# Kernel tuning notes

Measured on AMD Instinct MI355X. Metric: run time of the kernel, lower is better.

The kernel has to match this reference:

```python
import jax, jax.numpy as jnp
import numpy as np

S, B_BOX, C = 7, 2, 20
LAMBDA_COORD = 5.0
LAMBDA_NOOBJ = 0.5


def _iou(b1, b2):
    # b1, b2: [..., 4] in (cx, cy, w, h) format
    area1 = b1[..., 2] * b1[..., 3]
    area2 = b2[..., 2] * b2[..., 3]
    max_left = jnp.maximum(b1[..., 0] - b1[..., 2] / 2, b2[..., 0] - b2[..., 2] / 2)
    min_right = jnp.minimum(b1[..., 0] + b1[..., 2] / 2, b2[..., 0] + b2[..., 2] / 2)
    max_top = jnp.maximum(b1[..., 1] - b1[..., 3] / 2, b2[..., 1] - b2[..., 3] / 2)
    min_bottom = jnp.minimum(b1[..., 1] + b1[..., 3] / 2, b2[..., 1] + b2[..., 3] / 2)
    iw = jnp.maximum(min_right - max_left, 0.0)
    ih = jnp.maximum(min_bottom - max_top, 0.0)
    inter = iw * ih
    union = area1 + area2 - inter
    return jnp.where(inter > 0.0, inter / union, 0.0)


def setup_inputs() -> dict:
    key = jax.random.key(0)
    k1, k2, k3 = jax.random.split(key, 3)
    batch = 16384
    shape = (batch, S, S, C + 5 * B_BOX)  # [..., 30]
    pred = jax.random.uniform(k1, shape, dtype=jnp.float32)
    target = jax.random.uniform(k2, shape, dtype=jnp.float32)
    # objectness flag must be exactly 1.0 to trigger the obj branch
    obj_flag = jax.random.bernoulli(k3, 0.3, shape[:-1]).astype(jnp.float32)
    target = target.at[..., 0].set(obj_flag)
    return {"pred": pred, "target": target}


def reference(pred, target):
    batch = pred.shape[0]
    pred = pred.reshape(-1, S, S, C + 5 * B_BOX)
    target = target.reshape(-1, S, S, C + 5 * B_BOX)

    obj = (target[..., 0] == 1.0)          # [b,S,S] bool
    obj_f = obj.astype(pred.dtype)
    noobj_f = 1.0 - obj_f

    gt = target[..., 1:5]
    box1 = pred[..., 1:5]                   # predictor 1 box
    box2 = target[..., 6:10]                # NOTE: original code uses target's 2nd box
    iou1 = jax.lax.stop_gradient(_iou(box1, gt))
    iou2 = jax.lax.stop_gradient(_iou(box2, gt))
    resp1 = iou1 > iou2                     # predictor 1 responsible (strict >)
    r1 = resp1[..., None]

    # coord losses (responsible predictor)
    pxy = jnp.where(r1, pred[..., 1:3], pred[..., 6:8])
    txy = jnp.where(r1, target[..., 1:3], target[..., 6:8])
    pwh = jnp.where(r1, pred[..., 3:5], pred[..., 8:10])
    twh = jnp.where(r1, target[..., 3:5], target[..., 8:10])
    cell_xy = jnp.sum((pxy - txy) ** 2, axis=-1)
    cell_wh = jnp.sum((jnp.sqrt(pwh) - jnp.sqrt(twh)) ** 2, axis=-1)

    # obj confidence loss: responsible conf vs its iou
    conf_resp = jnp.where(resp1, pred[..., 0], pred[..., 5])
    iou_resp = jnp.where(resp1, iou1, iou2)
    cell_obj = (conf_resp - iou_resp) ** 2

    # noobj: non-responsible conf in obj cells; both confs in empty cells
    conf_other = jnp.where(resp1, pred[..., 5], pred[..., 0])
    cell_noobj_obj = conf_other ** 2
    cell_noobj_empty = pred[..., 0] ** 2 + pred[..., 5] ** 2

    cell_class = jnp.sum((pred[..., 10:] - target[..., 10:]) ** 2, axis=-1)

    loss_coord_xy = LAMBDA_COORD * jnp.sum(obj_f * cell_xy)
    loss_coord_wh = LAMBDA_COORD * jnp.sum(obj_f * cell_wh)
    loss_obj = jnp.sum(obj_f * cell_obj)
    loss_noobj = LAMBDA_NOOBJ * (jnp.sum(obj_f * cell_noobj_obj) + jnp.sum(noobj_f * cell_noobj_empty))
    loss_class = jnp.sum(obj_f * cell_class)
    loss = loss_coord_xy + loss_coord_wh + loss_obj + loss_noobj + loss_class

    bs = jnp.asarray(batch, pred.dtype)
    return ((loss_coord_xy + loss_coord_wh) / bs,
            loss_obj / bs,
            loss_noobj / bs,
            loss_class / bs,
            loss / bs)
```

## Files before the change

kernel.cpp:

```cpp
#include <hip/hip_runtime.h>

#define NCH 30
#define F2PC 15
#define TILE 64
#define TPB 64
#define MAXB 2560

typedef float fvec2 __attribute__((ext_vector_type(2)));
typedef float fvec4 __attribute__((ext_vector_type(4)));

__device__ __forceinline__ float iou_fn(float x1, float y1, float w1, float h1,
                                        float x2, float y2, float w2, float h2) {
    float a1 = w1 * h1, a2 = w2 * h2;
    float left  = fmaxf(x1 - w1 * 0.5f, x2 - w2 * 0.5f);
    float right = fminf(x1 + w1 * 0.5f, x2 + w2 * 0.5f);
    float top   = fmaxf(y1 - h1 * 0.5f, y2 - h2 * 0.5f);
    float bot   = fminf(y1 + h1 * 0.5f, y2 + h2 * 0.5f);
    float iw = fmaxf(right - left, 0.0f);
    float ih = fmaxf(bot - top, 0.0f);
    float inter = iw * ih;
    float uni = a1 + a2 - inter;
    return (inter > 0.0f) ? (inter / uni) : 0.0f;
}

__device__ __forceinline__ void cell_losses(const float* p, const float* t,
                                            float& coord, float& lobj,
                                            float& lnoobj, float& lclass) {
    float obj_f = (t[0] == 1.0f) ? 1.0f : 0.0f;

    float iou1 = iou_fn(p[1], p[2], p[3], p[4], t[1], t[2], t[3], t[4]);
    float iou2 = iou_fn(t[6], t[7], t[8], t[9], t[1], t[2], t[3], t[4]);
    bool r = iou1 > iou2;

    float px = r ? p[1] : p[6], py = r ? p[2] : p[7];
    float pw = r ? p[3] : p[8], ph = r ? p[4] : p[9];
    float tx = r ? t[1] : t[6], ty = r ? t[2] : t[7];
    float tw = r ? t[3] : t[8], th = r ? t[4] : t[9];

    float dx = px - tx, dy = py - ty;
    float cxy = dx * dx + dy * dy;
    float swv = sqrtf(pw) - sqrtf(tw), shv = sqrtf(ph) - sqrtf(th);
    float cwh = swv * swv + shv * shv;

    float conf_resp  = r ? p[0] : p[5];
    float iou_resp   = r ? iou1 : iou2;
    float conf_other = r ? p[5] : p[0];
    float dconf = conf_resp - iou_resp;

    coord  += obj_f * (cxy + cwh);
    lobj   += obj_f * dconf * dconf;
    lnoobj += obj_f * conf_other * conf_other
            + (1.0f - obj_f) * (p[0] * p[0] + p[5] * p[5]);

    float cls = 0.0f;
#pragma unroll
    for (int i = 10; i < NCH; i++) { float e = p[i] - t[i]; cls += e * e; }
    lclass += obj_f * cls;
}

#define LOADT(RP, RT, RP7, RT7, tile_) do {                                              \
    const long long b4_ = (long long)(tile_) * 480;                                      \
    _Pragma("unroll")                                                                    \
    for (int k_ = 0; k_ < 7; k_++) {                                                     \
        RP[k_] = __builtin_nontemporal_load(reinterpret_cast<const fvec4*>(pred) + b4_ + k_ * 64 + lane); \
        RT[k_] = __builtin_nontemporal_load(reinterpret_cast<const fvec4*>(targ) + b4_ + k_ * 64 + lane); \
    }                                                                                    \
    RP7 = __builtin_nontemporal_load(reinterpret_cast<const fvec2*>(pred) + 2 * b4_ + 896 + lane); \
    RT7 = __builtin_nontemporal_load(reinterpret_cast<const fvec2*>(targ) + 2 * b4_ + 896 + lane); \
} while (0)

#define STORE_LDS(RP, RT, RP7, RT7) do {                                                 \
    _Pragma("unroll")                                                                    \
    for (int k_ = 0; k_ < 7; k_++) {                                                     \
        sp4[k_ * 64 + lane] = RP[k_];                                                    \
        st4[k_ * 64 + lane] = RT[k_];                                                    \
    }                                                                                    \
    reinterpret_cast<fvec2*>(sp4)[896 + lane] = RP7;                                     \
    reinterpret_cast<fvec2*>(st4)[896 + lane] = RT7;                                     \
} while (0)

#define COMPUTE() do {                                                                   \
    float p_[NCH], t_[NCH];                                                              \
    const fvec2* pp_ = reinterpret_cast<const fvec2*>(sp4) + lane * F2PC;                \
    const fvec2* tp_ = reinterpret_cast<const fvec2*>(st4) + lane * F2PC;                \
    _Pragma("unroll")                                                                    \
    for (int k_ = 0; k_ < F2PC; k_++) { fvec2 v_ = pp_[k_]; p_[2 * k_] = v_.x; p_[2 * k_ + 1] = v_.y; } \
    _Pragma("unroll")                                                                    \
    for (int k_ = 0; k_ < F2PC; k_++) { fvec2 v_ = tp_[k_]; t_[2 * k_] = v_.x; t_[2 * k_ + 1] = v_.y; } \
    cell_losses(p_, t_, coord, lobj, lnoobj, lclass);                                    \
} while (0)

__global__ __launch_bounds__(TPB) void yolo_main(
        const float* __restrict__ pred, const float* __restrict__ targ,
        float4* __restrict__ partials, int n_full, int n_cells) {
    __shared__ fvec4 sp4[TILE * F2PC / 2];
    __shared__ fvec4 st4[TILE * F2PC / 2];

    const int lane = threadIdx.x;
    float coord = 0.f, lobj = 0.f, lnoobj = 0.f, lclass = 0.f;

    fvec4 rpA[7], rtA[7]; fvec2 rpA7, rtA7;
    fvec4 rpB[7], rtB[7]; fvec2 rpB7, rtB7;

    const int stride = gridDim.x;
    int tc = blockIdx.x;

    if (tc < n_full)              LOADT(rpA, rtA, rpA7, rtA7, tc);
    if (tc + stride < n_full)     LOADT(rpB, rtB, rpB7, rtB7, tc + stride);

    for (;;) {
        if (tc >= n_full) break;
        __syncthreads();
        STORE_LDS(rpA, rtA, rpA7, rtA7);
        if (tc + 2 * stride < n_full)
            LOADT(rpA, rtA, rpA7, rtA7, tc + 2 * stride);
        __syncthreads();
        COMPUTE();
        tc += stride;

        if (tc >= n_full) break;
        __syncthreads();
        STORE_LDS(rpB, rtB, rpB7, rtB7);
        if (tc + 2 * stride < n_full)
            LOADT(rpB, rtB, rpB7, rtB7, tc + 2 * stride);
        __syncthreads();
        COMPUTE();
        tc += stride;
    }

    if (blockIdx.x == 0) {
        int cell = n_full * TILE + lane;
        if (cell < n_cells) {
            float p[NCH], tt[NCH];
            const fvec2* pp = reinterpret_cast<const fvec2*>(pred) + (long long)cell * F2PC;
            const fvec2* tp = reinterpret_cast<const fvec2*>(targ) + (long long)cell * F2PC;
#pragma unroll
            for (int k = 0; k < F2PC; k++) { fvec2 v = pp[k]; p[2 * k] = v.x; p[2 * k + 1] = v.y; }
#pragma unroll
            for (int k = 0; k < F2PC; k++) { fvec2 v = tp[k]; tt[2 * k] = v.x; tt[2 * k + 1] = v.y; }
            cell_losses(p, tt, coord, lobj, lnoobj, lclass);
        }
    }

#pragma unroll
    for (int off = 32; off > 0; off >>= 1) {
        coord  += __shfl_down(coord, off);
        lobj   += __shfl_down(lobj, off);
        lnoobj += __shfl_down(lnoobj, off);
        lclass += __shfl_down(lclass, off);
    }
    if (lane == 0) partials[blockIdx.x] = make_float4(coord, lobj, lnoobj, lclass);
}

__global__ __launch_bounds__(256) void yolo_reduce(
        const float4* __restrict__ partials, int nparts,
        float* __restrict__ out, double inv_bs) {
    double s0 = 0.0, s1 = 0.0, s2 = 0.0, s3 = 0.0;
    for (int i = threadIdx.x; i < nparts; i += 256) {
        float4 v = partials[i];
        s0 += (double)v.x; s1 += (double)v.y;
        s2 += (double)v.z; s3 += (double)v.w;
    }
#pragma unroll
    for (int off = 32; off > 0; off >>= 1) {
        s0 += __shfl_down(s0, off);
        s1 += __shfl_down(s1, off);
        s2 += __shfl_down(s2, off);
        s3 += __shfl_down(s3, off);
    }
    __shared__ double red[4][4];
    int lane = threadIdx.x & 63;
    int wid  = threadIdx.x >> 6;
    if (lane == 0) {
        red[wid][0] = s0; red[wid][1] = s1;
        red[wid][2] = s2; red[wid][3] = s3;
    }
    __syncthreads();
    if (threadIdx.x == 0) {
        double a0 = 0, a1 = 0, a2 = 0, a3 = 0;
        for (int w = 0; w < 4; w++) {
            a0 += red[w][0]; a1 += red[w][1];
            a2 += red[w][2]; a3 += red[w][3];
        }
        double cd = a0 * 5.0 * inv_bs;
        double o  = a1 * inv_bs;
        double n  = a2 * 0.5 * inv_bs;
        double cl = a3 * inv_bs;
        out[0] = (float)cd;
        out[1] = (float)o;
        out[2] = (float)n;
        out[3] = (float)cl;
        out[4] = (float)(cd + o + n + cl);
    }
}

extern "C" void kernel_launch(void* const* d_in, const int* in_sizes, int n_in,
                              void* d_out, int out_size, void* d_ws, size_t ws_size,
                              hipStream_t stream) {
    const float* pred = (const float*)d_in[0];
    const float* targ = (const float*)d_in[1];
    float* out = (float*)d_out;
    float4* partials = (float4*)d_ws;

    int n_cells = in_sizes[0] / NCH;
    int batch   = n_cells / 49;
    int n_full  = n_cells / TILE;

    int grid = (n_full < 1) ? 1 : (n_full < MAXB ? n_full : MAXB);

    int max_parts = (int)(ws_size / sizeof(float4));
    if (max_parts >= 1 && grid > max_parts) grid = max_parts;

    yolo_main<<<grid, TPB, 0, stream>>>(pred, targ, partials, n_full, n_cells);
    yolo_reduce<<<1, 256, 0, stream>>>(partials, grid, out, 1.0 / (double)batch);
}
```

Measured before the change: 196.0 us.

## Load tiles directly into LDS with global_load_lds and drop block barriers

Result: faster. 191.8 us (-2.2%).

```diff
diff --git a/kernel.cpp b/kernel.cpp
--- a/kernel.cpp
+++ b/kernel.cpp
@@ -4,7 +4,7 @@
 #define F2PC 15
 #define TILE 64
 #define TPB 64
-#define MAXB 2560
+#define MAXB 1280
 
 typedef float fvec2 __attribute__((ext_vector_type(2)));
 typedef float fvec4 __attribute__((ext_vector_type(4)));
@@ -58,31 +58,37 @@
     lclass += obj_f * cls;
 }
 
-#define LOADT(RP, RT, RP7, RT7, tile_) do {                                              \
+#define GLDS16(gp, lp)                                                                   \
+    __builtin_amdgcn_global_load_lds(                                                    \
+        (const __attribute__((address_space(1))) void*)(gp),                             \
+        (__attribute__((address_space(3))) void*)(lp), 16, 0, 2)
+
+#define ISSUE_TILE(buf, tile_) do {                                                      \
     const long long b4_ = (long long)(tile_) * 480;                                      \
+    const fvec4* gp_ = reinterpret_cast<const fvec4*>(pred) + b4_;                       \
+    const fvec4* gt_ = reinterpret_cast<const fvec4*>(targ) + b4_;                       \
     _Pragma("unroll")                                                                    \
     for (int k_ = 0; k_ < 7; k_++) {                                                     \
-        RP[k_] = __builtin_nontemporal_load(reinterpret_cast<const fvec4*>(pred) + b4_ + k_ * 64 + lane); \
-        RT[k_] = __builtin_nontemporal_load(reinterpret_cast<const fvec4*>(targ) + b4_ + k_ * 64 + lane); \
+        GLDS16(gp_ + k_ * 64 + lane, &sbuf[buf][0][k_ * 64]);                            \
+        GLDS16(gt_ + k_ * 64 + lane, &sbuf[buf][1][k_ * 64]);                            \
     }                                                                                    \
-    RP7 = __builtin_nontemporal_load(reinterpret_cast<const fvec2*>(pred) + 2 * b4_ + 896 + lane); \
-    RT7 = __builtin_nontemporal_load(reinterpret_cast<const fvec2*>(targ) + 2 * b4_ + 896 + lane); \
+    if (lane < 32) {                                                                     \
+        GLDS16(gp_ + 448 + lane, &sbuf[buf][0][448]);                                    \
+        GLDS16(gt_ + 448 + lane, &sbuf[buf][1][448]);                                    \
+    }                                                                                    \
 } while (0)
 
-#define STORE_LDS(RP, RT, RP7, RT7) do {                                                 \
-    _Pragma("unroll")                                                                    \
-    for (int k_ = 0; k_ < 7; k_++) {                                                     \
-        sp4[k_ * 64 + lane] = RP[k_];                                                    \
-        st4[k_ * 64 + lane] = RT[k_];                                                    \
-    }                                                                                    \
-    reinterpret_cast<fvec2*>(sp4)[896 + lane] = RP7;                                     \
-    reinterpret_cast<fvec2*>(st4)[896 + lane] = RT7;                                     \
-} while (0)
-
-#define COMPUTE() do {                                                                   \
+#define WAITV16 do { asm volatile("s_waitcnt vmcnt(16)" ::: "memory"); \
+                     __builtin_amdgcn_sched_barrier(0); } while (0)
+#define WAITV0  do { asm volatile("s_waitcnt vmcnt(0)"  ::: "memory"); \
+                     __builtin_amdgcn_sched_barrier(0); } while (0)
+#define LDS_REUSE_GUARD do { asm volatile("s_waitcnt lgkmcnt(0)" ::: "memory"); \
+                             __builtin_amdgcn_sched_barrier(0); } while (0)
+
+#define COMPUTE(buf) do {                                                                \
     float p_[NCH], t_[NCH];                                                              \
-    const fvec2* pp_ = reinterpret_cast<const fvec2*>(sp4) + lane * F2PC;                \
-    const fvec2* tp_ = reinterpret_cast<const fvec2*>(st4) + lane * F2PC;                \
+    const fvec2* pp_ = reinterpret_cast<const fvec2*>(&sbuf[buf][0][0]) + lane * F2PC;   \
+    const fvec2* tp_ = reinterpret_cast<const fvec2*>(&sbuf[buf][1][0]) + lane * F2PC;   \
     _Pragma("unroll")                                                                    \
     for (int k_ = 0; k_ < F2PC; k_++) { fvec2 v_ = pp_[k_]; p_[2 * k_] = v_.x; p_[2 * k_ + 1] = v_.y; } \
     _Pragma("unroll")                                                                    \
@@ -93,38 +99,30 @@
 __global__ __launch_bounds__(TPB) void yolo_main(
         const float* __restrict__ pred, const float* __restrict__ targ,
         float4* __restrict__ partials, int n_full, int n_cells) {
-    __shared__ fvec4 sp4[TILE * F2PC / 2];
-    __shared__ fvec4 st4[TILE * F2PC / 2];
+    __shared__ fvec4 sbuf[2][2][480];
 
     const int lane = threadIdx.x;
     float coord = 0.f, lobj = 0.f, lnoobj = 0.f, lclass = 0.f;
 
-    fvec4 rpA[7], rtA[7]; fvec2 rpA7, rtA7;
-    fvec4 rpB[7], rtB[7]; fvec2 rpB7, rtB7;
-
     const int stride = gridDim.x;
     int tc = blockIdx.x;
 
-    if (tc < n_full)              LOADT(rpA, rtA, rpA7, rtA7, tc);
-    if (tc + stride < n_full)     LOADT(rpB, rtB, rpB7, rtB7, tc + stride);
+    if (tc < n_full)          ISSUE_TILE(0, tc);
+    if (tc + stride < n_full) ISSUE_TILE(1, tc + stride);
 
     for (;;) {
         if (tc >= n_full) break;
-        __syncthreads();
-        STORE_LDS(rpA, rtA, rpA7, rtA7);
-        if (tc + 2 * stride < n_full)
-            LOADT(rpA, rtA, rpA7, rtA7, tc + 2 * stride);
-        __syncthreads();
-        COMPUTE();
+        if (tc + stride < n_full) { WAITV16; } else { WAITV0; }
+        COMPUTE(0);
+        LDS_REUSE_GUARD;
+        if (tc + 2 * stride < n_full) ISSUE_TILE(0, tc + 2 * stride);
         tc += stride;
 
         if (tc >= n_full) break;
-        __syncthreads();
-        STORE_LDS(rpB, rtB, rpB7, rtB7);
-        if (tc + 2 * stride < n_full)
-            LOADT(rpB, rtB, rpB7, rtB7, tc + 2 * stride);
-        __syncthreads();
-        COMPUTE();
+        if (tc + stride < n_full) { WAITV16; } else { WAITV0; }
+        COMPUTE(1);
+        LDS_REUSE_GUARD;
+        if (tc + 2 * stride < n_full) ISSUE_TILE(1, tc + 2 * stride);
         tc += stride;
     }
 
```
